# Kernel optimization log

Measured on AMD Instinct MI355X. Metric: run time of the kernel, lower is better.

The kernel has to match this reference:

```python
import jax, jax.numpy as jnp
import numpy as np

DK = 64  # head dim = n_features // n_heads = 512 // 8


def setup_inputs() -> dict:
    key = jax.random.key(0)
    ks = jax.random.split(key, 6)
    B, N, D = 2, 4096, 512
    feature = jax.random.normal(ks[0], (B, N, D), dtype=jnp.float32)
    Sh = jax.random.normal(ks[1], (B, N, N), dtype=jnp.float32)
    Sw = jax.random.normal(ks[2], (B, N, N), dtype=jnp.float32)
    # torch Linear weights are [out, in]; xavier-uniform init
    lim = np.sqrt(6.0 / (D + DK)).astype(np.float32)
    wq_w = jax.random.uniform(ks[3], (DK, D), jnp.float32, -lim, lim)
    wk_w = jax.random.uniform(ks[4], (DK, D), jnp.float32, -lim, lim)
    wv_w = jax.random.uniform(ks[5], (DK, D), jnp.float32, -lim, lim)
    zb = jnp.zeros((DK,), jnp.float32)
    return {"feature": feature, "Sh": Sh, "Sw": Sw,
            "wq_w": wq_w, "wq_b": zb, "wk_w": wk_w, "wk_b": zb,
            "wv_w": wv_w, "wv_b": zb}


def reference(feature, Sh, Sw, wq_w, wq_b, wk_w, wk_b, wv_w, wv_b):
    # Linear projections (torch: x @ W.T + b)
    Q = jnp.einsum('bnd,kd->bnk', feature, wq_w) + wq_b  # [B,N,dk]
    K = jnp.einsum('bnd,kd->bnk', feature, wk_w) + wk_b  # [B,N,dk]
    V = jnp.einsum('bnd,kd->bnk', feature, wv_w) + wv_b  # [B,N,dv]
    sqrt_dk = jnp.sqrt(jnp.float32(Q.shape[-1]))
    # scores = (QK^T + Sh + Sw) / sqrt(dk)  -- biases added BEFORE scaling,
    # exactly as in attnFunc
    A = (jnp.einsum('bqk,bnk->bqn', Q, K) + Sh + Sw) / sqrt_dk  # [B,N,N]
    A = jax.nn.softmax(A, axis=-1)
    return jnp.einsum('bqn,bnk->bqk', A, V)  # [B,N,dv]
```

## Files before the change

kernel.cpp:

```cpp
#include <hip/hip_runtime.h>
#include <hip/hip_bf16.h>


typedef short bf16x8 __attribute__((ext_vector_type(8)));
typedef short bf16x4 __attribute__((ext_vector_type(4)));
typedef float f32x4  __attribute__((ext_vector_type(4)));

#if __has_builtin(__builtin_amdgcn_exp2f)
#define EXP2F(x) __builtin_amdgcn_exp2f(x)
#else
#define EXP2F(x) exp2f(x)
#endif

__device__ __forceinline__ f32x4 mfma16(bf16x8 a, bf16x8 b, f32x4 c) {
  return __builtin_amdgcn_mfma_f32_16x16x32_bf16(a, b, c, 0, 0, 0);
}
__device__ __forceinline__ short f2b(float x) {
  __hip_bfloat16 h = __float2bfloat16(x);
  return __builtin_bit_cast(short, h);
}
__device__ __forceinline__ float b2f(short s) {
  return __bfloat162float(__builtin_bit_cast(__hip_bfloat16, s));
}
__device__ __forceinline__ void split_hl(float x, short& h, short& l) {
  __hip_bfloat16 bh = __float2bfloat16(x);
  h = __builtin_bit_cast(short, bh);
  l = f2b(x - __bfloat162float(bh));
}

__global__ void wcvt_kernel(const float* __restrict__ wq, const float* __restrict__ wk,
                            const float* __restrict__ wv,
                            short* __restrict__ wh, short* __restrict__ wl) {
  int idx = (blockIdx.x * 256 + threadIdx.x) * 4;
  int p = idx >> 15;
  int off = idx & 32767;
  const float* src = (p == 0) ? wq : (p == 1) ? wk : wv;
  f32x4 v = *(const f32x4*)(src + off);
  bf16x4 h, l;
#pragma unroll
  for (int j = 0; j < 4; ++j) { short hh, ll; split_hl(v[j], hh, ll); h[j] = hh; l[j] = ll; }
  *(bf16x4*)(wh + p * 32768 + off) = h;
  *(bf16x4*)(wl + p * 32768 + off) = l;
}

__global__ __launch_bounds__(64) void proj_kernel(
    const float* __restrict__ feat, const short* __restrict__ wh, const short* __restrict__ wl,
    const float* __restrict__ bq, const float* __restrict__ bk, const float* __restrict__ bv,
    short* __restrict__ Qh, short* __restrict__ Ql,
    short* __restrict__ Kh, short* __restrict__ Kl, short* __restrict__ Vt) {
  int lane = threadIdx.x & 63;
  int lq = lane & 15, quad = lane >> 4;
  int rbase = blockIdx.x * 16;
  f32x4 acc[3][4];
#pragma unroll
  for (int p = 0; p < 3; ++p)
#pragma unroll
    for (int t = 0; t < 4; ++t) acc[p][t] = (f32x4){0.f, 0.f, 0.f, 0.f};

  const float* frow = feat + (size_t)(rbase + lq) * 512 + quad * 8;
  for (int ks = 0; ks < 16; ++ks) {
    f32x4 f0 = *(const f32x4*)(frow + ks * 32);
    f32x4 f1 = *(const f32x4*)(frow + ks * 32 + 4);
    bf16x8 fh, fl;
#pragma unroll
    for (int j = 0; j < 4; ++j) {
      short hh, ll;
      split_hl(f0[j], hh, ll); fh[j] = hh; fl[j] = ll;
      split_hl(f1[j], hh, ll); fh[j + 4] = hh; fl[j + 4] = ll;
    }
#pragma unroll
    for (int p = 0; p < 3; ++p)
#pragma unroll
      for (int t = 0; t < 4; ++t) {
        const int wo = (p * 64 + t * 16 + lq) * 512 + ks * 32 + quad * 8;
        bf16x8 wfh = *(const bf16x8*)(wh + wo);
        bf16x8 wfl = *(const bf16x8*)(wl + wo);
        acc[p][t] = mfma16(fh, wfh, acc[p][t]);
        acc[p][t] = mfma16(fl, wfh, acc[p][t]);
        acc[p][t] = mfma16(fh, wfl, acc[p][t]);
      }
  }
  int b = rbase >> 12;
  int rloc = rbase & 4095;
#pragma unroll
  for (int t = 0; t < 4; ++t) {
    int dk = t * 16 + lq;
    float bqv = bq[dk], bkv = bk[dk], bvv = bv[dk];
    bf16x4 vpack;
#pragma unroll
    for (int r = 0; r < 4; ++r) {
      int row = rbase + 4 * quad + r;
      short h, l;
      split_hl(acc[0][t][r] + bqv, h, l);
      Qh[row * 64 + dk] = h; Ql[row * 64 + dk] = l;
      split_hl(acc[1][t][r] + bkv, h, l);
      Kh[row * 64 + dk] = h; Kl[row * 64 + dk] = l;
      vpack[r] = f2b(acc[2][t][r] + bvv);
    }
    *(bf16x4*)(Vt + (size_t)(b * 64 + dk) * 4096 + rloc + 4 * quad) = vpack;
  }
}

__global__ __launch_bounds__(256, 4) void attn_kernel(
    const float* __restrict__ Sh, const float* __restrict__ Sw,
    const short* __restrict__ Qh, const short* __restrict__ Ql,
    const short* __restrict__ Kh, const short* __restrict__ Kl,
    const short* __restrict__ Vt,
    float* __restrict__ Opart, float* __restrict__ lpart) {
  __shared__ short Plds[4][16][40];
  const int bid = blockIdx.x;
  const int sp = bid & 7, qt = (bid >> 3) & 63, b = bid >> 9;
  const int tid = threadIdx.x;
  const int wave = tid >> 6, lane = tid & 63, lq = lane & 15, quad = lane >> 4;
  const int qbase = qt * 64 + wave * 16;

  bf16x8 qfh[2], qfl[2];
  {
    const int qidx = (b * 4096 + qbase + lq) * 64 + quad * 8;
    qfh[0] = *(const bf16x8*)(Qh + qidx);
    qfh[1] = *(const bf16x8*)(Qh + qidx + 32);
    qfl[0] = *(const bf16x8*)(Ql + qidx);
    qfl[1] = *(const bf16x8*)(Ql + qidx + 32);
  }
  f32x4 accO[4];
#pragma unroll
  for (int u = 0; u < 4; ++u) accO[u] = (f32x4){0.f, 0.f, 0.f, 0.f};
  float lsum[4] = {0.f, 0.f, 0.f, 0.f};
  const float Cs = 0.18033688011112042f;
  const size_t biasRow = (size_t)(b * 4096 + qbase + 4 * quad) * 4096;
  short* pw = &Plds[wave][0][0];

  for (int it = 0; it < 16; ++it) {
    const int kb = sp * 512 + it * 32;
    f32x4 accS[2];
    accS[0] = (f32x4){0.f, 0.f, 0.f, 0.f};
    accS[1] = (f32x4){0.f, 0.f, 0.f, 0.f};
#pragma unroll
    for (int t = 0; t < 2; ++t) {
      const int kidx = (b * 4096 + kb + t * 16 + lq) * 64 + quad * 8;
      bf16x8 kh0 = *(const bf16x8*)(Kh + kidx);
      bf16x8 kh1 = *(const bf16x8*)(Kh + kidx + 32);
      bf16x8 kl0 = *(const bf16x8*)(Kl + kidx);
      bf16x8 kl1 = *(const bf16x8*)(Kl + kidx + 32);
      accS[t] = mfma16(qfh[0], kh0, accS[t]);
      accS[t] = mfma16(qfh[1], kh1, accS[t]);
      accS[t] = mfma16(qfl[0], kh0, accS[t]);
      accS[t] = mfma16(qfl[1], kh1, accS[t]);
      accS[t] = mfma16(qfh[0], kl0, accS[t]);
      accS[t] = mfma16(qfh[1], kl1, accS[t]);
    }
#pragma unroll
    for (int t = 0; t < 2; ++t) {
#pragma unroll
      for (int r = 0; r < 4; ++r) {
        const size_t bi = biasRow + (size_t)r * 4096 + (kb + t * 16 + lq);
        float s = accS[t][r] + __builtin_nontemporal_load(Sh + bi)
                            + __builtin_nontemporal_load(Sw + bi);
        float p = EXP2F(s * Cs);
        lsum[r] += p;
        pw[(4 * quad + r) * 40 + t * 16 + lq] = f2b(p);
      }
    }
    bf16x8 pa = *(const bf16x8*)(pw + lq * 40 + quad * 8);
#pragma unroll
    for (int u = 0; u < 4; ++u) {
      const bf16x8 vf = *(const bf16x8*)(Vt + (size_t)(b * 64 + u * 16 + lq) * 4096 + kb + quad * 8);
      accO[u] = mfma16(pa, vf, accO[u]);
    }
  }
#pragma unroll
  for (int r = 0; r < 4; ++r)
#pragma unroll
    for (int m = 1; m < 16; m <<= 1) lsum[r] += __shfl_xor(lsum[r], m, 64);

  const int orow = sp * 8192 + b * 4096 + qbase + 4 * quad;
#pragma unroll
  for (int r = 0; r < 4; ++r) {
#pragma unroll
    for (int u = 0; u < 4; ++u)
      Opart[(size_t)(orow + r) * 64 + u * 16 + lq] = accO[u][r];
    if (lq == 0) lpart[orow + r] = lsum[r];
  }
}

__global__ void combine_kernel(const float* __restrict__ Opart, const float* __restrict__ lpart,
                               float* __restrict__ out) {
  int g = blockIdx.x * 256 + threadIdx.x;
  int row = g >> 6;
  float o = 0.f, l = 0.f;
#pragma unroll
  for (int s = 0; s < 8; ++s) {
    o += __builtin_nontemporal_load(Opart + (size_t)s * 524288 + g);
    l += lpart[s * 8192 + row];
  }
  out[g] = o / l;
}

extern "C" void kernel_launch(void* const* d_in, const int* in_sizes, int n_in,
                              void* d_out, int out_size, void* d_ws, size_t ws_size,
                              hipStream_t stream) {
  const float* feature = (const float*)d_in[0];
  const float* Sh = (const float*)d_in[1];
  const float* Sw = (const float*)d_in[2];
  const float* wq = (const float*)d_in[3];
  const float* bq = (const float*)d_in[4];
  const float* wk = (const float*)d_in[5];
  const float* bk = (const float*)d_in[6];
  const float* wv = (const float*)d_in[7];
  const float* bv = (const float*)d_in[8];

  char* ws = (char*)d_ws;
  const size_t MB = 1u << 20;
  short* Qh = (short*)(ws + 0 * MB);
  short* Ql = (short*)(ws + 1 * MB);
  short* Kh = (short*)(ws + 2 * MB);
  short* Kl = (short*)(ws + 3 * MB);
  short* Vt = (short*)(ws + 4 * MB);
  short* wh = (short*)(ws + 5 * MB);
  short* wl = (short*)(ws + 5 * MB + 262144);
  float* lpart = (float*)(ws + 5 * MB + 524288);
  float* Opart = (float*)(ws + 6 * MB);

  wcvt_kernel<<<96, 256, 0, stream>>>(wq, wk, wv, wh, wl);
  proj_kernel<<<512, 64, 0, stream>>>(feature, wh, wl, bq, bk, bv, Qh, Ql, Kh, Kl, Vt);
  attn_kernel<<<1024, 256, 0, stream>>>(Sh, Sw, Qh, Ql, Kh, Kl, Vt, Opart, lpart);
  combine_kernel<<<2048, 256, 0, stream>>>(Opart, lpart, (float*)d_out);
}
```

Before: 411.0 us.

## Transpose score MFMA for vectorized bias loads and widen key tile

Computes the score tile transposed so each lane owns four consecutive key columns of a query row, which allows 16-byte vector loads of the Sh/Sw bias matrices instead of scalar strided loads. The attention loop now processes 64 keys per iteration and issues all K and bias loads before the MFMAs. The softmax scale is folded into Q in the projection, the projection is split into one wave per Q/K/V output, and the combine kernel is vectorized with a reciprocal. This raises register pressure from the larger prefetch and introduces a slight rounding difference from pre-scaling Q.

```diff
diff --git a/kernel.cpp b/kernel.cpp
--- a/kernel.cpp
+++ b/kernel.cpp
@@ -11,6 +11,11 @@
 #else
 #define EXP2F(x) exp2f(x)
 #endif
+#if __has_builtin(__builtin_amdgcn_rcpf)
+#define RCPF(x) __builtin_amdgcn_rcpf(x)
+#else
+#define RCPF(x) (1.0f / (x))
+#endif
 
 __device__ __forceinline__ f32x4 mfma16(bf16x8 a, bf16x8 b, f32x4 c) {
   return __builtin_amdgcn_mfma_f32_16x16x32_bf16(a, b, c, 0, 0, 0);
@@ -18,9 +23,6 @@
 __device__ __forceinline__ short f2b(float x) {
   __hip_bfloat16 h = __float2bfloat16(x);
   return __builtin_bit_cast(short, h);
-}
-__device__ __forceinline__ float b2f(short s) {
-  return __bfloat162float(__builtin_bit_cast(__hip_bfloat16, s));
 }
 __device__ __forceinline__ void split_hl(float x, short& h, short& l) {
   __hip_bfloat16 bh = __float2bfloat16(x);
@@ -43,21 +45,24 @@
   *(bf16x4*)(wl + p * 32768 + off) = l;
 }
 
-__global__ __launch_bounds__(64) void proj_kernel(
+__global__ __launch_bounds__(256) void proj_kernel(
     const float* __restrict__ feat, const short* __restrict__ wh, const short* __restrict__ wl,
     const float* __restrict__ bq, const float* __restrict__ bk, const float* __restrict__ bv,
     short* __restrict__ Qh, short* __restrict__ Ql,
     short* __restrict__ Kh, short* __restrict__ Kl, short* __restrict__ Vt) {
-  int lane = threadIdx.x & 63;
-  int lq = lane & 15, quad = lane >> 4;
-  int rbase = blockIdx.x * 16;
-  f32x4 acc[3][4];
-#pragma unroll
-  for (int p = 0; p < 3; ++p)
-#pragma unroll
-    for (int t = 0; t < 4; ++t) acc[p][t] = (f32x4){0.f, 0.f, 0.f, 0.f};
+  const int lane = threadIdx.x & 63, wave = threadIdx.x >> 6;
+  const int lq = lane & 15, quad = lane >> 4;
+  const int wid = blockIdx.x * 4 + wave;
+  const int p = wid >> 9, rg = wid & 511;
+  const int rbase = rg * 16;
+  const float Cs = 0.18033688011112042f;
+
+  f32x4 acc[4];
+#pragma unroll
+  for (int t = 0; t < 4; ++t) acc[t] = (f32x4){0.f, 0.f, 0.f, 0.f};
 
   const float* frow = feat + (size_t)(rbase + lq) * 512 + quad * 8;
+  const int wrow = p * 64;
   for (int ks = 0; ks < 16; ++ks) {
     f32x4 f0 = *(const f32x4*)(frow + ks * 32);
     f32x4 f1 = *(const f32x4*)(frow + ks * 32 + 4);
@@ -69,35 +74,52 @@
       split_hl(f1[j], hh, ll); fh[j + 4] = hh; fl[j + 4] = ll;
     }
 #pragma unroll
-    for (int p = 0; p < 3; ++p)
-#pragma unroll
-      for (int t = 0; t < 4; ++t) {
-        const int wo = (p * 64 + t * 16 + lq) * 512 + ks * 32 + quad * 8;
-        bf16x8 wfh = *(const bf16x8*)(wh + wo);
-        bf16x8 wfl = *(const bf16x8*)(wl + wo);
-        acc[p][t] = mfma16(fh, wfh, acc[p][t]);
-        acc[p][t] = mfma16(fl, wfh, acc[p][t]);
-        acc[p][t] = mfma16(fh, wfl, acc[p][t]);
-      }
-  }
-  int b = rbase >> 12;
-  int rloc = rbase & 4095;
-#pragma unroll
-  for (int t = 0; t < 4; ++t) {
-    int dk = t * 16 + lq;
-    float bqv = bq[dk], bkv = bk[dk], bvv = bv[dk];
-    bf16x4 vpack;
-#pragma unroll
-    for (int r = 0; r < 4; ++r) {
-      int row = rbase + 4 * quad + r;
-      short h, l;
-      split_hl(acc[0][t][r] + bqv, h, l);
-      Qh[row * 64 + dk] = h; Ql[row * 64 + dk] = l;
-      split_hl(acc[1][t][r] + bkv, h, l);
-      Kh[row * 64 + dk] = h; Kl[row * 64 + dk] = l;
-      vpack[r] = f2b(acc[2][t][r] + bvv);
-    }
-    *(bf16x4*)(Vt + (size_t)(b * 64 + dk) * 4096 + rloc + 4 * quad) = vpack;
+    for (int t = 0; t < 4; ++t) {
+      const int wo = (wrow + t * 16 + lq) * 512 + ks * 32 + quad * 8;
+      bf16x8 wfh = *(const bf16x8*)(wh + wo);
+      bf16x8 wfl = *(const bf16x8*)(wl + wo);
+      acc[t] = mfma16(fh, wfh, acc[t]);
+      acc[t] = mfma16(fl, wfh, acc[t]);
+      acc[t] = mfma16(fh, wfl, acc[t]);
+    }
+  }
+  const int b = rbase >> 12, rloc = rbase & 4095;
+  if (p == 0) {
+#pragma unroll
+    for (int t = 0; t < 4; ++t) {
+      const int dk = t * 16 + lq;
+      const float bb = bq[dk];
+#pragma unroll
+      for (int r = 0; r < 4; ++r) {
+        const int row = rbase + 4 * quad + r;
+        short h, l;
+        split_hl((acc[t][r] + bb) * Cs, h, l);
+        Qh[row * 64 + dk] = h; Ql[row * 64 + dk] = l;
+      }
+    }
+  } else if (p == 1) {
+#pragma unroll
+    for (int t = 0; t < 4; ++t) {
+      const int dk = t * 16 + lq;
+      const float bb = bk[dk];
+#pragma unroll
+      for (int r = 0; r < 4; ++r) {
+        const int row = rbase + 4 * quad + r;
+        short h, l;
+        split_hl(acc[t][r] + bb, h, l);
+        Kh[row * 64 + dk] = h; Kl[row * 64 + dk] = l;
+      }
+    }
+  } else {
+#pragma unroll
+    for (int t = 0; t < 4; ++t) {
+      const int dk = t * 16 + lq;
+      const float bb = bv[dk];
+      bf16x4 vpack;
+#pragma unroll
+      for (int r = 0; r < 4; ++r) vpack[r] = f2b(acc[t][r] + bb);
+      *(bf16x4*)(Vt + (size_t)(b * 64 + dk) * 4096 + rloc + 4 * quad) = vpack;
+    }
   }
 }
 
@@ -107,93 +129,105 @@
     const short* __restrict__ Kh, const short* __restrict__ Kl,
     const short* __restrict__ Vt,
     float* __restrict__ Opart, float* __restrict__ lpart) {
-  __shared__ short Plds[4][16][40];
+  __shared__ short Plds[4][16][72];
   const int bid = blockIdx.x;
   const int sp = bid & 7, qt = (bid >> 3) & 63, b = bid >> 9;
   const int tid = threadIdx.x;
   const int wave = tid >> 6, lane = tid & 63, lq = lane & 15, quad = lane >> 4;
   const int qbase = qt * 64 + wave * 16;
-
-  bf16x8 qfh[2], qfl[2];
-  {
-    const int qidx = (b * 4096 + qbase + lq) * 64 + quad * 8;
-    qfh[0] = *(const bf16x8*)(Qh + qidx);
-    qfh[1] = *(const bf16x8*)(Qh + qidx + 32);
-    qfl[0] = *(const bf16x8*)(Ql + qidx);
-    qfl[1] = *(const bf16x8*)(Ql + qidx + 32);
-  }
+  const float Cs = 0.18033688011112042f;
+
+  const int qidx = (b * 4096 + qbase + lq) * 64 + quad * 8;
+  const bf16x8 qfh0 = *(const bf16x8*)(Qh + qidx);
+  const bf16x8 qfh1 = *(const bf16x8*)(Qh + qidx + 32);
+  const bf16x8 qfl0 = *(const bf16x8*)(Ql + qidx);
+  const bf16x8 qfl1 = *(const bf16x8*)(Ql + qidx + 32);
+
   f32x4 accO[4];
 #pragma unroll
   for (int u = 0; u < 4; ++u) accO[u] = (f32x4){0.f, 0.f, 0.f, 0.f};
-  float lsum[4] = {0.f, 0.f, 0.f, 0.f};
-  const float Cs = 0.18033688011112042f;
-  const size_t biasRow = (size_t)(b * 4096 + qbase + 4 * quad) * 4096;
+  float lsum = 0.f;
+  const size_t qrowOff = (size_t)(b * 4096 + qbase + lq) * 4096;
   short* pw = &Plds[wave][0][0];
-
-  for (int it = 0; it < 16; ++it) {
-    const int kb = sp * 512 + it * 32;
-    f32x4 accS[2];
-    accS[0] = (f32x4){0.f, 0.f, 0.f, 0.f};
-    accS[1] = (f32x4){0.f, 0.f, 0.f, 0.f};
-#pragma unroll
-    for (int t = 0; t < 2; ++t) {
+  const short* vbase = Vt + (size_t)b * 64 * 4096;
+
+  for (int it = 0; it < 8; ++it) {
+    const int kb = sp * 512 + it * 64;
+    bf16x8 kh0[4], kh1[4], kl0[4], kl1[4];
+#pragma unroll
+    for (int t = 0; t < 4; ++t) {
       const int kidx = (b * 4096 + kb + t * 16 + lq) * 64 + quad * 8;
-      bf16x8 kh0 = *(const bf16x8*)(Kh + kidx);
-      bf16x8 kh1 = *(const bf16x8*)(Kh + kidx + 32);
-      bf16x8 kl0 = *(const bf16x8*)(Kl + kidx);
-      bf16x8 kl1 = *(const bf16x8*)(Kl + kidx + 32);
-      accS[t] = mfma16(qfh[0], kh0, accS[t]);
-      accS[t] = mfma16(qfh[1], kh1, accS[t]);
-      accS[t] = mfma16(qfl[0], kh0, accS[t]);
-      accS[t] = mfma16(qfl[1], kh1, accS[t]);
-      accS[t] = mfma16(qfh[0], kl0, accS[t]);
-      accS[t] = mfma16(qfh[1], kl1, accS[t]);
-    }
-#pragma unroll
-    for (int t = 0; t < 2; ++t) {
+      kh0[t] = *(const bf16x8*)(Kh + kidx);
+      kh1[t] = *(const bf16x8*)(Kh + kidx + 32);
+      kl0[t] = *(const bf16x8*)(Kl + kidx);
+      kl1[t] = *(const bf16x8*)(Kl + kidx + 32);
+    }
+    f32x4 bsh[4], bsw[4];
+#pragma unroll
+    for (int t = 0; t < 4; ++t) {
+      const size_t bi = qrowOff + kb + 16 * t + 4 * quad;
+      bsh[t] = __builtin_nontemporal_load((const f32x4*)(Sh + bi));
+      bsw[t] = __builtin_nontemporal_load((const f32x4*)(Sw + bi));
+    }
+    f32x4 accS[4];
+#pragma unroll
+    for (int t = 0; t < 4; ++t) accS[t] = (f32x4){0.f, 0.f, 0.f, 0.f};
+#pragma unroll
+    for (int t = 0; t < 4; ++t) {
+      accS[t] = mfma16(kh0[t], qfh0, accS[t]);
+      accS[t] = mfma16(kh1[t], qfh1, accS[t]);
+      accS[t] = mfma16(kh0[t], qfl0, accS[t]);
+      accS[t] = mfma16(kh1[t], qfl1, accS[t]);
+      accS[t] = mfma16(kl0[t], qfh0, accS[t]);
+      accS[t] = mfma16(kl1[t], qfh1, accS[t]);
+    }
+#pragma unroll
+    for (int t = 0; t < 4; ++t) {
+      bf16x4 pk;
 #pragma unroll
       for (int r = 0; r < 4; ++r) {
-        const size_t bi = biasRow + (size_t)r * 4096 + (kb + t * 16 + lq);
-        float s = accS[t][r] + __builtin_nontemporal_load(Sh + bi)
-                            + __builtin_nontemporal_load(Sw + bi);
-        float p = EXP2F(s * Cs);
-        lsum[r] += p;
-        pw[(4 * quad + r) * 40 + t * 16 + lq] = f2b(p);
-      }
-    }
-    bf16x8 pa = *(const bf16x8*)(pw + lq * 40 + quad * 8);
-#pragma unroll
-    for (int u = 0; u < 4; ++u) {
-      const bf16x8 vf = *(const bf16x8*)(Vt + (size_t)(b * 64 + u * 16 + lq) * 4096 + kb + quad * 8);
-      accO[u] = mfma16(pa, vf, accO[u]);
-    }
-  }
-#pragma unroll
-  for (int r = 0; r < 4; ++r)
-#pragma unroll
-    for (int m = 1; m < 16; m <<= 1) lsum[r] += __shfl_xor(lsum[r], m, 64);
-
-  const int orow = sp * 8192 + b * 4096 + qbase + 4 * quad;
-#pragma unroll
-  for (int r = 0; r < 4; ++r) {
-#pragma unroll
-    for (int u = 0; u < 4; ++u)
-      Opart[(size_t)(orow + r) * 64 + u * 16 + lq] = accO[u][r];
-    if (lq == 0) lpart[orow + r] = lsum[r];
-  }
+        float s = fmaf(bsh[t][r] + bsw[t][r], Cs, accS[t][r]);
+        float p = EXP2F(s);
+        lsum += p;
+        pk[r] = f2b(p);
+      }
+      *(bf16x4*)(pw + lq * 72 + 16 * t + 4 * quad) = pk;
+    }
+#pragma unroll
+    for (int c = 0; c < 2; ++c) {
+      const bf16x8 pa = *(const bf16x8*)(pw + lq * 72 + c * 32 + quad * 8);
+#pragma unroll
+      for (int u = 0; u < 4; ++u) {
+        const bf16x8 vf = *(const bf16x8*)(vbase + (size_t)(u * 16 + lq) * 4096 + kb + c * 32 + quad * 8);
+        accO[u] = mfma16(pa, vf, accO[u]);
+      }
+    }
+  }
+  lsum += __shfl_xor(lsum, 16, 64);
+  lsum += __shfl_xor(lsum, 32, 64);
+
+  const int orowW = sp * 8192 + b * 4096 + qbase;
+  if (quad == 0) lpart[orowW + lq] = lsum;
+#pragma unroll
+  for (int u = 0; u < 4; ++u)
+#pragma unroll
+    for (int r = 0; r < 4; ++r)
+      Opart[(size_t)(orowW + 4 * quad + r) * 64 + u * 16 + lq] = accO[u][r];
 }
 
 __global__ void combine_kernel(const float* __restrict__ Opart, const float* __restrict__ lpart,
                                float* __restrict__ out) {
-  int g = blockIdx.x * 256 + threadIdx.x;
-  int row = g >> 6;
-  float o = 0.f, l = 0.f;
+  const int g = blockIdx.x * 256 + threadIdx.x;
+  const int row = g >> 4;
+  f32x4 o = (f32x4){0.f, 0.f, 0.f, 0.f};
+  float l = 0.f;
 #pragma unroll
   for (int s = 0; s < 8; ++s) {
-    o += __builtin_nontemporal_load(Opart + (size_t)s * 524288 + g);
+    o += __builtin_nontemporal_load((const f32x4*)(Opart + (size_t)s * 524288 + g * 4));
     l += lpart[s * 8192 + row];
   }
-  out[g] = o / l;
+  const float rl = RCPF(l);
+  *(f32x4*)(out + g * 4) = o * rl;
 }
 
 extern "C" void kernel_launch(void* const* d_in, const int* in_sizes, int n_in,
@@ -222,7 +256,7 @@
   float* Opart = (float*)(ws + 6 * MB);
 
   wcvt_kernel<<<96, 256, 0, stream>>>(wq, wk, wv, wh, wl);
-  proj_kernel<<<512, 64, 0, stream>>>(feature, wh, wl, bq, bk, bv, Qh, Ql, Kh, Kl, Vt);
+  proj_kernel<<<384, 256, 0, stream>>>(feature, wh, wl, bq, bk, bv, Qh, Ql, Kh, Kl, Vt);
   attn_kernel<<<1024, 256, 0, stream>>>(Sh, Sw, Qh, Ql, Kh, Kl, Vt, Opart, lpart);
-  combine_kernel<<<2048, 256, 0, stream>>>(Opart, lpart, (float*)d_out);
-}
+  combine_kernel<<<512, 256, 0, stream>>>(Opart, lpart, (float*)d_out);
+}
```

New measurement: 398.5 us. 3.0% less time.
